# Performance work log

Hardware: AMD Instinct MI355X
Metric: run time of the kernel (lower is better)

The kernel has to match this reference:

```python
import jax, jax.numpy as jnp
import numpy as np

B, N_VEC, N_DIM, N_W, N_HID, VOCAB, N_CLASS = 16, 2048, 32, 4, 128, 32000, 10


def setup_inputs() -> dict:
    key = jax.random.key(0)
    ks = jax.random.split(key, 8)
    data = jax.random.randint(ks[0], (B, N_VEC), 0, VOCAB, dtype=jnp.int64)
    emb = jax.random.normal(ks[1], (VOCAB, N_DIM), dtype=jnp.float32) * 0.1
    # stacked per-layer weights for the n_W WModules: Linear(n_dim->n_hid), GELU, Linear(n_hid->n_vec)
    fw1 = jax.random.normal(ks[2], (N_W, N_DIM, N_HID), dtype=jnp.float32) * (1.0 / np.sqrt(N_DIM))
    fb1 = jnp.zeros((N_W, N_HID), dtype=jnp.float32)
    fw2 = jax.random.normal(ks[3], (N_W, N_HID, N_VEC), dtype=jnp.float32) * (1.0 / np.sqrt(N_HID))
    fb2 = jnp.zeros((N_W, N_VEC), dtype=jnp.float32)
    Wf = jax.random.normal(ks[4], (N_VEC * N_DIM, N_CLASS), dtype=jnp.float32) * (1.0 / np.sqrt(N_VEC * N_DIM))
    bf = jnp.zeros((N_CLASS,), dtype=jnp.float32)
    return {"data": data, "emb": emb, "fw1": fw1, "fb1": fb1, "fw2": fw2, "fb2": fb2, "Wf": Wf, "bf": bf}


def reference(data, emb, fw1, fb1, fw2, fb2, Wf, bf):
    X = emb[data]                       # [B, n_vec, n_dim]
    V = X                               # g is identity (with_g=False)
    # iterate over self.fs[::-1]: indices n_W-1 .. 0
    for i in range(N_W - 1, -1, -1):
        h = jax.nn.gelu(jnp.einsum('bnd,dh->bnh', X, fw1[i]) + fb1[i], approximate=False)
        W = jnp.einsum('bnh,hm->bnm', h, fw2[i]) + fb2[i]   # [B, n_vec, n_vec]
        V = jnp.einsum('bnm,bmd->bnd', W, V)                # [B, n_vec, n_dim]
    out = V.reshape(V.shape[0], -1) @ Wf + bf               # [B, n_class]
    return out
```

## Files before the change

### kernel.cpp

```cpp
#include <hip/hip_runtime.h>

#define NB 16
#define NVEC 2048
#define NDIM 32
#define NW 4
#define NHID 128
#define NCLASS 10
#define NG 32
#define USIZE (129 * 32)

__device__ __forceinline__ float gelu_fast(float x) {
    float t = 1.5957691216057308f * x * (1.0f + 0.044715f * x * x);
    return x / (1.0f + __expf(-t));
}

__device__ __forceinline__ void upart_phase(const float* __restrict__ vs,
                                            const float* __restrict__ fw2s,
                                            const float* __restrict__ fb2l,
                                            int n0, int tid,
                                            float* __restrict__ Up) {
    int kg = tid & 31, d0 = (tid >> 5) * 4;
    float acc[4][4];
#pragma unroll
    for (int i = 0; i < 4; ++i)
#pragma unroll
        for (int j = 0; j < 4; ++j) acc[i][j] = 0.f;
#pragma unroll 4
    for (int mm = 0; mm < 64; mm += 4) {
        float4 w[4], v[4];
#pragma unroll
        for (int i = 0; i < 4; ++i)
            w[i] = *(const float4*)&fw2s[(kg + 32 * i) * 68 + mm];
#pragma unroll
        for (int j = 0; j < 4; ++j)
            v[j] = *(const float4*)&vs[(mm + j) * 36 + d0];
#pragma unroll
        for (int i = 0; i < 4; ++i) {
            const float* wf = (const float*)&w[i];
#pragma unroll
            for (int j = 0; j < 4; ++j) {
                float wv = wf[j];
                acc[i][0] += wv * v[j].x; acc[i][1] += wv * v[j].y;
                acc[i][2] += wv * v[j].z; acc[i][3] += wv * v[j].w;
            }
        }
    }
#pragma unroll
    for (int i = 0; i < 4; ++i)
        *(float4*)&Up[(kg + 32 * i) * 32 + d0] =
            make_float4(acc[i][0], acc[i][1], acc[i][2], acc[i][3]);
    if (tid < 32) {
        float ca = 0.f;
#pragma unroll 8
        for (int mm = 0; mm < 64; ++mm)
            ca += fb2l[n0 + mm] * vs[mm * 36 + tid];
        Up[128 * 32 + tid] = ca;
    }
}

__global__ __launch_bounds__(256) void k_emb(const int* __restrict__ data,
                                             const float* __restrict__ emb,
                                             const float* __restrict__ fw2l,
                                             const float* __restrict__ fb2l,
                                             const float* __restrict__ bf,
                                             float* __restrict__ X,
                                             float* __restrict__ Upart,
                                             float* __restrict__ out) {
    __shared__ float vs[64 * 36];
    __shared__ float fw2s[128 * 68];
    int ng = blockIdx.x, b = blockIdx.y, tid = threadIdx.x;
    int n0 = ng * 64;
#pragma unroll
    for (int j = 0; j < 2; ++j) {
        int i = tid + j * 256;
        int r = i >> 3, c4 = (i & 7) * 4;
        int idx = data[b * NVEC + n0 + r];
        float4 v = *(const float4*)&emb[(size_t)idx * NDIM + c4];
        *(float4*)&vs[r * 36 + c4] = v;
        *(float4*)&X[((size_t)b * NVEC + n0 + r) * NDIM + c4] = v;
    }
#pragma unroll
    for (int j = 0; j < 8; ++j) {
        int i = tid + j * 256;
        int k = i >> 4, c4 = (i & 15) * 4;
        *(float4*)&fw2s[k * 68 + c4] =
            *(const float4*)&fw2l[(size_t)k * NVEC + n0 + c4];
    }
    if (ng == 0 && b == 0 && tid < NB * NCLASS)
        out[tid] = bf[tid % NCLASS];
    __syncthreads();
    upart_phase(vs, fw2s, fb2l, n0, tid, Upart + ((size_t)ng * NB + b) * USIZE);
}

__global__ __launch_bounds__(256) void k_Ured(const float* __restrict__ Upart,
                                              float* __restrict__ U) {
    int b = blockIdx.x;
    int i4 = blockIdx.y * 256 + threadIdx.x;
    if (i4 >= USIZE / 4) return;
    float4 s = ((const float4*)(Upart + (size_t)b * USIZE))[i4];
#pragma unroll
    for (int ms = 1; ms < NG; ++ms) {
        float4 v = ((const float4*)(Upart + ((size_t)ms * NB + b) * USIZE))[i4];
        s.x += v.x; s.y += v.y; s.z += v.z; s.w += v.w;
    }
    ((float4*)(U + (size_t)b * USIZE))[i4] = s;
}

template <bool LAST>
__global__ __launch_bounds__(256) void k_apply(const float* __restrict__ X,
                                               const float* __restrict__ fw1l,
                                               const float* __restrict__ fb1l,
                                               const float* __restrict__ U,
                                               const float* __restrict__ fw2n,
                                               const float* __restrict__ fb2n,
                                               float* __restrict__ Upart,
                                               const float* __restrict__ Wf,
                                               float* __restrict__ out) {
    __shared__ float xs[64 * 36];
    __shared__ float w1s[32 * 132];
    __shared__ float hsb[128 * 68];
    __shared__ float Us[USIZE];
    __shared__ float ored[4][NCLASS];
    int ng = blockIdx.x, b = blockIdx.y, tid = threadIdx.x;
    int n0 = ng * 64;

#pragma unroll
    for (int j = 0; j < 2; ++j) {
        int i = tid + j * 256;
        int r = i >> 3, c4 = (i & 7) * 4;
        *(float4*)&xs[r * 36 + c4] =
            *(const float4*)&X[((size_t)b * NVEC + n0 + r) * NDIM + c4];
    }
#pragma unroll
    for (int j = 0; j < 4; ++j) {
        int i = tid + j * 256;
        int d = i >> 5, c4 = (i & 31) * 4;
        *(float4*)&w1s[d * 132 + c4] = *(const float4*)&fw1l[d * NHID + c4];
    }
    for (int i4 = tid; i4 < USIZE / 4; i4 += 256)
        ((float4*)Us)[i4] = ((const float4*)(U + (size_t)b * USIZE))[i4];
    __syncthreads();

    int rg = tid & 31;
    {
        int k0 = (tid >> 5) * 16;
        float acc[2][16];
        {
            float4 bq[4];
#pragma unroll
            for (int q = 0; q < 4; ++q) bq[q] = *(const float4*)&fb1l[k0 + 4 * q];
#pragma unroll
            for (int q = 0; q < 4; ++q) {
                acc[0][4 * q + 0] = bq[q].x; acc[0][4 * q + 1] = bq[q].y;
                acc[0][4 * q + 2] = bq[q].z; acc[0][4 * q + 3] = bq[q].w;
                acc[1][4 * q + 0] = bq[q].x; acc[1][4 * q + 1] = bq[q].y;
                acc[1][4 * q + 2] = bq[q].z; acc[1][4 * q + 3] = bq[q].w;
            }
        }
#pragma unroll 4
        for (int d = 0; d < NDIM; ++d) {
            float x0 = xs[rg * 36 + d];
            float x1 = xs[(rg + 32) * 36 + d];
            const float* wrow = &w1s[d * 132 + k0];
            float4 w0 = *(const float4*)wrow;
            float4 w1 = *(const float4*)(wrow + 4);
            float4 w2 = *(const float4*)(wrow + 8);
            float4 w3 = *(const float4*)(wrow + 12);
            float wk[16] = {w0.x, w0.y, w0.z, w0.w, w1.x, w1.y, w1.z, w1.w,
                            w2.x, w2.y, w2.z, w2.w, w3.x, w3.y, w3.z, w3.w};
#pragma unroll
            for (int j = 0; j < 16; ++j) {
                acc[0][j] += x0 * wk[j];
                acc[1][j] += x1 * wk[j];
            }
        }
#pragma unroll
        for (int r = 0; r < 2; ++r) {
            int row = rg + 32 * r;
#pragma unroll
            for (int q = 0; q < 4; ++q) {
                float4 o;
                o.x = gelu_fast(acc[r][4 * q + 0]);
                o.y = gelu_fast(acc[r][4 * q + 1]);
                o.z = gelu_fast(acc[r][4 * q + 2]);
                o.w = gelu_fast(acc[r][4 * q + 3]);
                *(float4*)&hsb[row * 132 + k0 + 4 * q] = o;
            }
        }
    }
    __syncthreads();

    int dg = (tid >> 5) & 3, kh = tid >> 7;
    int d0 = dg * 8, kb = kh * 64;
    float a[2][8];
#pragma unroll
    for (int r = 0; r < 2; ++r)
#pragma unroll
        for (int j = 0; j < 8; ++j) a[r][j] = 0.f;
#pragma unroll 4
    for (int ks = 0; ks < 64; ks += 4) {
        int kk = kb + ks;
        float4 h0 = *(const float4*)&hsb[rg * 132 + kk];
        float4 h1 = *(const float4*)&hsb[(rg + 32) * 132 + kk];
        float4 u[4][2];
#pragma unroll
        for (int j = 0; j < 4; ++j) {
            u[j][0] = *(const float4*)&Us[(kk + j) * 32 + d0];
            u[j][1] = *(const float4*)&Us[(kk + j) * 32 + d0 + 4];
        }
        const float* hf0 = (const float*)&h0;
        const float* hf1 = (const float*)&h1;
#pragma unroll
        for (int j = 0; j < 4; ++j) {
            float v0 = hf0[j], v1 = hf1[j];
            a[0][0] += v0 * u[j][0].x; a[0][1] += v0 * u[j][0].y;
            a[0][2] += v0 * u[j][0].z; a[0][3] += v0 * u[j][0].w;
            a[0][4] += v0 * u[j][1].x; a[0][5] += v0 * u[j][1].y;
            a[0][6] += v0 * u[j][1].z; a[0][7] += v0 * u[j][1].w;
            a[1][0] += v1 * u[j][0].x; a[1][1] += v1 * u[j][0].y;
            a[1][2] += v1 * u[j][0].z; a[1][3] += v1 * u[j][0].w;
            a[1][4] += v1 * u[j][1].x; a[1][5] += v1 * u[j][1].y;
            a[1][6] += v1 * u[j][1].z; a[1][7] += v1 * u[j][1].w;
        }
    }
    if (kh == 1) {
#pragma unroll
        for (int r = 0; r < 2; ++r) {
            float* p = &xs[(rg + 32 * r) * 36 + d0];
            *(float4*)p       = make_float4(a[r][0], a[r][1], a[r][2], a[r][3]);
            *(float4*)(p + 4) = make_float4(a[r][4], a[r][5], a[r][6], a[r][7]);
        }
    }
    __syncthreads();

    if constexpr (!LAST) {
#pragma unroll
        for (int j = 0; j < 8; ++j) {
            int i = tid + j * 256;
            int k = i >> 4, c4 = (i & 15) * 4;
            *(float4*)&hsb[k * 68 + c4] =
                *(const float4*)&fw2n[(size_t)k * NVEC + n0 + c4];
        }
    }
    if (kh == 0) {
        float4 ub0 = *(const float4*)&Us[128 * 32 + d0];
        float4 ub1 = *(const float4*)&Us[128 * 32 + d0 + 4];
#pragma unroll
        for (int r = 0; r < 2; ++r) {
            float* p = &xs[(rg + 32 * r) * 36 + d0];
            float4 p0 = *(const float4*)p;
            float4 p1 = *(const float4*)(p + 4);
            a[r][0] += p0.x + ub0.x; a[r][1] += p0.y + ub0.y;
            a[r][2] += p0.z + ub0.z; a[r][3] += p0.w + ub0.w;
            a[r][4] += p1.x + ub1.x; a[r][5] += p1.y + ub1.y;
            a[r][6] += p1.z + ub1.z; a[r][7] += p1.w + ub1.w;
            *(float4*)p       = make_float4(a[r][0], a[r][1], a[r][2], a[r][3]);
            *(float4*)(p + 4) = make_float4(a[r][4], a[r][5], a[r][6], a[r][7]);
        }
    }
    __syncthreads();

    if constexpr (!LAST) {
        upart_phase(xs, hsb, fb2n, n0, tid,
                    Upart + ((size_t)ng * NB + b) * USIZE);
    } else {
        float accC[NCLASS];
#pragma unroll
        for (int c = 0; c < NCLASS; ++c) accC[c] = 0.f;
        if (kh == 0) {
#pragma unroll
            for (int r = 0; r < 2; ++r) {
                int nrow = n0 + rg + 32 * r;
#pragma unroll
                for (int dd = 0; dd < 8; ++dd) {
                    float v = a[r][dd];
                    const float2* wr =
                        (const float2*)(Wf + ((size_t)nrow * 32 + d0 + dd) * NCLASS);
#pragma unroll
                    for (int p = 0; p < 5; ++p) {
                        float2 w = wr[p];
                        accC[2 * p]     += v * w.x;
                        accC[2 * p + 1] += v * w.y;
                    }
                }
            }
        }
#pragma unroll
        for (int c = 0; c < NCLASS; ++c)
#pragma unroll
            for (int off = 32; off >= 1; off >>= 1)
                accC[c] += __shfl_down(accC[c], off, 64);
        int w = tid >> 6;
        if ((tid & 63) == 0) {
#pragma unroll
            for (int c = 0; c < NCLASS; ++c) ored[w][c] = accC[c];
        }
        __syncthreads();
        if (tid < NCLASS)
            atomicAdd(&out[b * NCLASS + tid],
                      ored[0][tid] + ored[1][tid] + ored[2][tid] + ored[3][tid]);
    }
}

extern "C" void kernel_launch(void* const* d_in, const int* in_sizes, int n_in,
                              void* d_out, int out_size, void* d_ws, size_t ws_size,
                              hipStream_t stream) {
    const int*   data = (const int*)d_in[0];
    const float* emb  = (const float*)d_in[1];
    const float* fw1  = (const float*)d_in[2];
    const float* fb1  = (const float*)d_in[3];
    const float* fw2  = (const float*)d_in[4];
    const float* fb2  = (const float*)d_in[5];
    const float* Wf   = (const float*)d_in[6];
    const float* bf   = (const float*)d_in[7];
    float* out = (float*)d_out;

    float* X     = (float*)d_ws;
    float* Upart = X + (size_t)NB * NVEC * NDIM;
    float* U     = Upart + (size_t)NG * NB * USIZE;

    k_emb<<<dim3(NG, NB), 256, 0, stream>>>(data, emb, fw2 + 3 * (size_t)NHID * NVEC,
                                            fb2 + 3 * (size_t)NVEC, bf, X, Upart, out);
    k_Ured<<<dim3(NB, 5), 256, 0, stream>>>(Upart, U);

    for (int i = NW - 1; i >= 1; --i) {
        k_apply<false><<<dim3(NG, NB), 256, 0, stream>>>(
            X, fw1 + (size_t)i * NDIM * NHID, fb1 + (size_t)i * NHID, U,
            fw2 + (size_t)(i - 1) * NHID * NVEC, fb2 + (size_t)(i - 1) * NVEC,
            Upart, nullptr, nullptr);
        k_Ured<<<dim3(NB, 5), 256, 0, stream>>>(Upart, U);
    }
    k_apply<true><<<dim3(NG, NB), 256, 0, stream>>>(
        X, fw1, fb1, U, nullptr, nullptr, nullptr, Wf, out);
}
```

Baseline: 176.0 us.

## Reassociate layer chain into independent 129x129 transfer matrices computed in parallel

Exploits the fact that each layer applies W_i = h_i(X) fw2_i, with X fixed, so the product fw2_j·H_{j+1} can be formed as a small 129x129 augmented matrix per layer and batch. All layers are computed in one parallel kernel instead of a serial apply/reduce chain, then composed with a tiny chain kernel before the final layer. This removes the sequential dependency and cuts the launch count, at the price of extra workspace and more FLOPs spent on the 129x129 transfer matrices.

Result: slower. 198.2 us (+12.6%).

```diff
diff --git a/kernel.cpp b/kernel.cpp
--- a/kernel.cpp
+++ b/kernel.cpp
@@ -6,139 +6,311 @@
 #define NW 4
 #define NHID 128
 #define NCLASS 10
-#define NG 32
-#define USIZE (129 * 32)
+#define TPSZ (129 * 132)
+#define TP4  (TPSZ / 4)
+#define USZ  (129 * 32)
+#define U4   (USZ / 4)
 
 __device__ __forceinline__ float gelu_fast(float x) {
     float t = 1.5957691216057308f * x * (1.0f + 0.044715f * x * x);
     return x / (1.0f + __expf(-t));
 }
 
-__device__ __forceinline__ void upart_phase(const float* __restrict__ vs,
-                                            const float* __restrict__ fw2s,
-                                            const float* __restrict__ fb2l,
-                                            int n0, int tid,
-                                            float* __restrict__ Up) {
-    int kg = tid & 31, d0 = (tid >> 5) * 4;
-    float acc[4][4];
-#pragma unroll
-    for (int i = 0; i < 4; ++i)
-#pragma unroll
-        for (int j = 0; j < 4; ++j) acc[i][j] = 0.f;
+__global__ __launch_bounds__(256) void k_big(const int* __restrict__ data,
+                                             const float* __restrict__ emb,
+                                             const float* __restrict__ fw1,
+                                             const float* __restrict__ fb1,
+                                             const float* __restrict__ fw2,
+                                             const float* __restrict__ fb2,
+                                             float* __restrict__ X,
+                                             float* __restrict__ Tpart,
+                                             float* __restrict__ U3part) {
+    __shared__ float hbuf[128 * 132];
+    __shared__ float fb2s[128];
+    int tid = threadIdx.x, bx = blockIdx.x;
+
+    if (bx < 256) {
+        int b = bx >> 4, chunk = bx & 15, m0 = chunk * 128;
+        const float* fw2l = fw2 + 3 * (size_t)NHID * NVEC;
+        float* xs = hbuf;
+#pragma unroll
+        for (int jj = 0; jj < 4; ++jj) {
+            int i4 = tid + jj * 256;
+            int r = i4 >> 3, c4 = (i4 & 7) * 4;
+            int idx = data[b * NVEC + m0 + r];
+            float4 v = *(const float4*)&emb[(size_t)idx * NDIM + c4];
+            *(float4*)&xs[r * 36 + c4] = v;
+            *(float4*)&X[((size_t)b * NVEC + m0 + r) * NDIM + c4] = v;
+        }
+        if (tid < 128) fb2s[tid] = fb2[3 * NVEC + m0 + tid];
+        __syncthreads();
+        int kg = tid & 31, d0 = (tid >> 5) * 4;
+        float acc[4][4];
+#pragma unroll
+        for (int i = 0; i < 4; ++i)
+#pragma unroll
+            for (int q = 0; q < 4; ++q) acc[i][q] = 0.f;
+        for (int mm = 0; mm < 128; mm += 4) {
+            float4 w[4], v[4];
+#pragma unroll
+            for (int i = 0; i < 4; ++i)
+                w[i] = *(const float4*)&fw2l[(size_t)(kg + 32 * i) * NVEC + m0 + mm];
+#pragma unroll
+            for (int q = 0; q < 4; ++q)
+                v[q] = *(const float4*)&xs[(mm + q) * 36 + d0];
+#pragma unroll
+            for (int i = 0; i < 4; ++i) {
+                const float* wf = (const float*)&w[i];
+#pragma unroll
+                for (int q = 0; q < 4; ++q) {
+                    float wv = wf[q];
+                    acc[i][0] += wv * v[q].x; acc[i][1] += wv * v[q].y;
+                    acc[i][2] += wv * v[q].z; acc[i][3] += wv * v[q].w;
+                }
+            }
+        }
+        float* Up = U3part + (size_t)(b * 16 + chunk) * USZ;
+#pragma unroll
+        for (int i = 0; i < 4; ++i)
+            *(float4*)&Up[(kg + 32 * i) * 32 + d0] =
+                make_float4(acc[i][0], acc[i][1], acc[i][2], acc[i][3]);
+        if (tid < 32) {
+            float ca = 0.f;
+#pragma unroll 8
+            for (int mm = 0; mm < 128; ++mm) ca += fb2s[mm] * xs[mm * 36 + tid];
+            Up[128 * 32 + tid] = ca;
+        }
+    } else {
+        int t = bx - 256;
+        int j = t >> 8, rr = t & 255;
+        int b = rr >> 4, chunk = rr & 15, m0 = chunk * 128;
+        const float* w1l  = fw1 + (size_t)(j + 1) * NDIM * NHID;
+        const float* b1l  = fb1 + (size_t)(j + 1) * NHID;
+        const float* fw2l = fw2 + (size_t)j * NHID * NVEC;
+        float* xs  = hbuf;
+        float* w1s = hbuf + 128 * 33;
+#pragma unroll
+        for (int jj = 0; jj < 4; ++jj) {
+            int i4 = tid + jj * 256;
+            int r = i4 >> 3, c4 = (i4 & 7) * 4;
+            int idx = data[b * NVEC + m0 + r];
+            float4 v = *(const float4*)&emb[(size_t)idx * NDIM + c4];
+            xs[r * 33 + c4] = v.x; xs[r * 33 + c4 + 1] = v.y;
+            xs[r * 33 + c4 + 2] = v.z; xs[r * 33 + c4 + 3] = v.w;
+        }
+#pragma unroll
+        for (int jj = 0; jj < 4; ++jj) {
+            int i4 = tid + jj * 256;
+            int d = i4 >> 5, c4 = (i4 & 31) * 4;
+            *(float4*)&w1s[d * 132 + c4] = *(const float4*)&w1l[d * NHID + c4];
+        }
+        if (tid < 128) fb2s[tid] = fb2[(size_t)j * NVEC + m0 + tid];
+        __syncthreads();
+
+        int rg = tid & 31, kg = tid >> 5, k0 = kg * 16;
+        float hr[4][16];
+        {
+            float4 bq[4];
+#pragma unroll
+            for (int q = 0; q < 4; ++q) bq[q] = *(const float4*)&b1l[k0 + 4 * q];
+#pragma unroll
+            for (int i = 0; i < 4; ++i)
+#pragma unroll
+                for (int q = 0; q < 4; ++q) {
+                    hr[i][4 * q]     = bq[q].x; hr[i][4 * q + 1] = bq[q].y;
+                    hr[i][4 * q + 2] = bq[q].z; hr[i][4 * q + 3] = bq[q].w;
+                }
+        }
 #pragma unroll 4
-    for (int mm = 0; mm < 64; mm += 4) {
-        float4 w[4], v[4];
+        for (int d = 0; d < NDIM; ++d) {
+            float xv[4];
+#pragma unroll
+            for (int i = 0; i < 4; ++i) xv[i] = xs[(rg + 32 * i) * 33 + d];
+            const float* wrow = &w1s[d * 132 + k0];
+            float4 w0 = *(const float4*)wrow;
+            float4 w1 = *(const float4*)(wrow + 4);
+            float4 w2 = *(const float4*)(wrow + 8);
+            float4 w3 = *(const float4*)(wrow + 12);
+            float wk[16] = {w0.x, w0.y, w0.z, w0.w, w1.x, w1.y, w1.z, w1.w,
+                            w2.x, w2.y, w2.z, w2.w, w3.x, w3.y, w3.z, w3.w};
+#pragma unroll
+            for (int i = 0; i < 4; ++i)
+#pragma unroll
+                for (int q = 0; q < 16; ++q) hr[i][q] += xv[i] * wk[q];
+        }
+        __syncthreads();
+#pragma unroll
+        for (int i = 0; i < 4; ++i) {
+            int row = rg + 32 * i;
+#pragma unroll
+            for (int q4 = 0; q4 < 4; ++q4) {
+                float4 o;
+                o.x = gelu_fast(hr[i][4 * q4]);     o.y = gelu_fast(hr[i][4 * q4 + 1]);
+                o.z = gelu_fast(hr[i][4 * q4 + 2]); o.w = gelu_fast(hr[i][4 * q4 + 3]);
+                *(float4*)&hbuf[row * 132 + k0 + 4 * q4] = o;
+            }
+            if (kg == 0) hbuf[row * 132 + 128] = 1.0f;
+        }
+        __syncthreads();
+
+        int pg = tid & 31, qg = tid >> 5, q0 = qg * 16;
+        float ta[4][16];
 #pragma unroll
         for (int i = 0; i < 4; ++i)
-            w[i] = *(const float4*)&fw2s[(kg + 32 * i) * 68 + mm];
-#pragma unroll
-        for (int j = 0; j < 4; ++j)
-            v[j] = *(const float4*)&vs[(mm + j) * 36 + d0];
-#pragma unroll
-        for (int i = 0; i < 4; ++i) {
-            const float* wf = (const float*)&w[i];
-#pragma unroll
-            for (int j = 0; j < 4; ++j) {
-                float wv = wf[j];
-                acc[i][0] += wv * v[j].x; acc[i][1] += wv * v[j].y;
-                acc[i][2] += wv * v[j].z; acc[i][3] += wv * v[j].w;
-            }
-        }
-    }
-#pragma unroll
-    for (int i = 0; i < 4; ++i)
-        *(float4*)&Up[(kg + 32 * i) * 32 + d0] =
-            make_float4(acc[i][0], acc[i][1], acc[i][2], acc[i][3]);
-    if (tid < 32) {
-        float ca = 0.f;
+#pragma unroll
+            for (int q = 0; q < 16; ++q) ta[i][q] = 0.f;
+        for (int mt = 0; mt < 128; mt += 8) {
+            float4 wr[4][2];
+#pragma unroll
+            for (int i = 0; i < 4; ++i) {
+                const float* wb = &fw2l[(size_t)(pg + 32 * i) * NVEC + m0 + mt];
+                wr[i][0] = *(const float4*)wb;
+                wr[i][1] = *(const float4*)(wb + 4);
+            }
+#pragma unroll
+            for (int m8 = 0; m8 < 8; ++m8) {
+                const float* hrow = &hbuf[(mt + m8) * 132 + q0];
+                float4 h0 = *(const float4*)hrow;
+                float4 h1 = *(const float4*)(hrow + 4);
+                float4 h2 = *(const float4*)(hrow + 8);
+                float4 h3 = *(const float4*)(hrow + 12);
+                float hv[16] = {h0.x, h0.y, h0.z, h0.w, h1.x, h1.y, h1.z, h1.w,
+                                h2.x, h2.y, h2.z, h2.w, h3.x, h3.y, h3.z, h3.w};
+#pragma unroll
+                for (int i = 0; i < 4; ++i) {
+                    float wv = ((const float*)&wr[i][m8 >> 2])[m8 & 3];
+#pragma unroll
+                    for (int q = 0; q < 16; ++q) ta[i][q] += wv * hv[q];
+                }
+            }
+        }
+        float* Tp = Tpart + (size_t)t * TPSZ;
+#pragma unroll
+        for (int i = 0; i < 4; ++i)
+#pragma unroll
+            for (int q4 = 0; q4 < 4; ++q4)
+                *(float4*)&Tp[(pg + 32 * i) * 132 + q0 + 4 * q4] =
+                    make_float4(ta[i][4 * q4], ta[i][4 * q4 + 1],
+                                ta[i][4 * q4 + 2], ta[i][4 * q4 + 3]);
+        if (tid < 128) {
+            float s = 0.f;
+            const float* wb = &fw2l[(size_t)tid * NVEC + m0];
 #pragma unroll 8
-        for (int mm = 0; mm < 64; ++mm)
-            ca += fb2l[n0 + mm] * vs[mm * 36 + tid];
-        Up[128 * 32 + tid] = ca;
-    }
-}
-
-__global__ __launch_bounds__(256) void k_emb(const int* __restrict__ data,
-                                             const float* __restrict__ emb,
-                                             const float* __restrict__ fw2l,
-                                             const float* __restrict__ fb2l,
-                                             const float* __restrict__ bf,
-                                             float* __restrict__ X,
-                                             float* __restrict__ Upart,
-                                             float* __restrict__ out) {
-    __shared__ float vs[64 * 36];
-    __shared__ float fw2s[128 * 68];
-    int ng = blockIdx.x, b = blockIdx.y, tid = threadIdx.x;
-    int n0 = ng * 64;
-#pragma unroll
-    for (int j = 0; j < 2; ++j) {
-        int i = tid + j * 256;
-        int r = i >> 3, c4 = (i & 7) * 4;
-        int idx = data[b * NVEC + n0 + r];
-        float4 v = *(const float4*)&emb[(size_t)idx * NDIM + c4];
-        *(float4*)&vs[r * 36 + c4] = v;
-        *(float4*)&X[((size_t)b * NVEC + n0 + r) * NDIM + c4] = v;
-    }
-#pragma unroll
-    for (int j = 0; j < 8; ++j) {
-        int i = tid + j * 256;
-        int k = i >> 4, c4 = (i & 15) * 4;
-        *(float4*)&fw2s[k * 68 + c4] =
-            *(const float4*)&fw2l[(size_t)k * NVEC + n0 + c4];
-    }
-    if (ng == 0 && b == 0 && tid < NB * NCLASS)
-        out[tid] = bf[tid % NCLASS];
-    __syncthreads();
-    upart_phase(vs, fw2s, fb2l, n0, tid, Upart + ((size_t)ng * NB + b) * USIZE);
-}
-
-__global__ __launch_bounds__(256) void k_Ured(const float* __restrict__ Upart,
-                                              float* __restrict__ U) {
-    int b = blockIdx.x;
-    int i4 = blockIdx.y * 256 + threadIdx.x;
-    if (i4 >= USIZE / 4) return;
-    float4 s = ((const float4*)(Upart + (size_t)b * USIZE))[i4];
-#pragma unroll
-    for (int ms = 1; ms < NG; ++ms) {
-        float4 v = ((const float4*)(Upart + ((size_t)ms * NB + b) * USIZE))[i4];
-        s.x += v.x; s.y += v.y; s.z += v.z; s.w += v.w;
-    }
-    ((float4*)(U + (size_t)b * USIZE))[i4] = s;
-}
-
-template <bool LAST>
-__global__ __launch_bounds__(256) void k_apply(const float* __restrict__ X,
-                                               const float* __restrict__ fw1l,
-                                               const float* __restrict__ fb1l,
-                                               const float* __restrict__ U,
-                                               const float* __restrict__ fw2n,
-                                               const float* __restrict__ fb2n,
-                                               float* __restrict__ Upart,
+            for (int mm = 0; mm < 128; mm += 4) {
+                float4 wq = *(const float4*)&wb[mm];
+                s += wq.x + wq.y + wq.z + wq.w;
+            }
+            Tp[tid * 132 + 128] = s;
+        }
+        if (tid < 129) {
+            float s = 0.f;
+#pragma unroll 8
+            for (int mm = 0; mm < 128; ++mm) s += fb2s[mm] * hbuf[mm * 132 + tid];
+            Tp[128 * 132 + tid] = s;
+        }
+    }
+}
+
+__global__ __launch_bounds__(256) void k_red(const float* __restrict__ Tpart,
+                                             const float* __restrict__ U3part,
+                                             float* __restrict__ Tfin,
+                                             float* __restrict__ U3fin) {
+    int x = blockIdx.x, y = blockIdx.y, tid = threadIdx.x;
+    if (y < 48) {
+        int i4 = x * 256 + tid;
+        if (i4 >= TP4) return;
+        float4 s = ((const float4*)Tpart)[(size_t)(y * 16) * TP4 + i4];
+#pragma unroll
+        for (int c = 1; c < 16; ++c) {
+            float4 v = ((const float4*)Tpart)[(size_t)(y * 16 + c) * TP4 + i4];
+            s.x += v.x; s.y += v.y; s.z += v.z; s.w += v.w;
+        }
+        ((float4*)Tfin)[(size_t)y * TP4 + i4] = s;
+    } else {
+        int b = y - 48;
+        int i4 = x * 256 + tid;
+        if (i4 >= U4) return;
+        float4 s = ((const float4*)U3part)[(size_t)(b * 16) * U4 + i4];
+#pragma unroll
+        for (int c = 1; c < 16; ++c) {
+            float4 v = ((const float4*)U3part)[(size_t)(b * 16 + c) * U4 + i4];
+            s.x += v.x; s.y += v.y; s.z += v.z; s.w += v.w;
+        }
+        ((float4*)U3fin)[(size_t)b * U4 + i4] = s;
+    }
+}
+
+__global__ __launch_bounds__(256) void k_chain(const float* __restrict__ Tfin,
+                                               const float* __restrict__ U3fin,
+                                               const float* __restrict__ bf,
+                                               float* __restrict__ U0,
+                                               float* __restrict__ out) {
+    __shared__ float Ul[2][129 * 4];
+    int dg = blockIdx.x, b = blockIdx.y, tid = threadIdx.x;
+    int d0 = dg * 4;
+    if (dg == 0 && tid < NCLASS) out[b * NCLASS + tid] = bf[tid];
+    if (tid < 129)
+        *(float4*)&Ul[0][tid * 4] =
+            *(const float4*)&U3fin[(size_t)b * USZ + tid * 32 + d0];
+    int cur = 0;
+    float4 acc = make_float4(0.f, 0.f, 0.f, 0.f);
+    for (int j = 2; j >= 0; --j) {
+        __syncthreads();
+        if (tid < 129) {
+            const float* rowp = Tfin + (size_t)(j * 16 + b) * TPSZ + tid * 132;
+            acc = make_float4(0.f, 0.f, 0.f, 0.f);
+            for (int r4 = 0; r4 < 32; ++r4) {
+                float4 tv = *(const float4*)&rowp[4 * r4];
+                float4 u0 = *(const float4*)&Ul[cur][(4 * r4 + 0) * 4];
+                float4 u1 = *(const float4*)&Ul[cur][(4 * r4 + 1) * 4];
+                float4 u2 = *(const float4*)&Ul[cur][(4 * r4 + 2) * 4];
+                float4 u3 = *(const float4*)&Ul[cur][(4 * r4 + 3) * 4];
+                acc.x += tv.x * u0.x + tv.y * u1.x + tv.z * u2.x + tv.w * u3.x;
+                acc.y += tv.x * u0.y + tv.y * u1.y + tv.z * u2.y + tv.w * u3.y;
+                acc.z += tv.x * u0.z + tv.y * u1.z + tv.z * u2.z + tv.w * u3.z;
+                acc.w += tv.x * u0.w + tv.y * u1.w + tv.z * u2.w + tv.w * u3.w;
+            }
+            float tl = rowp[128];
+            float4 ub = *(const float4*)&Ul[cur][128 * 4];
+            acc.x += tl * ub.x; acc.y += tl * ub.y;
+            acc.z += tl * ub.z; acc.w += tl * ub.w;
+        }
+        __syncthreads();
+        if (tid < 129) *(float4*)&Ul[cur ^ 1][tid * 4] = acc;
+        cur ^= 1;
+    }
+    if (tid < 129)
+        *(float4*)&U0[(size_t)b * USZ + tid * 32 + d0] = acc;
+}
+
+__global__ __launch_bounds__(256) void k_final(const float* __restrict__ X,
+                                               const float* __restrict__ fw1,
+                                               const float* __restrict__ fb1,
+                                               const float* __restrict__ U0,
                                                const float* __restrict__ Wf,
                                                float* __restrict__ out) {
     __shared__ float xs[64 * 36];
     __shared__ float w1s[32 * 132];
-    __shared__ float hsb[128 * 68];
-    __shared__ float Us[USIZE];
+    __shared__ float hs[64 * 132];
+    __shared__ float Us[USZ];
     __shared__ float ored[4][NCLASS];
     int ng = blockIdx.x, b = blockIdx.y, tid = threadIdx.x;
     int n0 = ng * 64;
-
-#pragma unroll
-    for (int j = 0; j < 2; ++j) {
-        int i = tid + j * 256;
-        int r = i >> 3, c4 = (i & 7) * 4;
+#pragma unroll
+    for (int jj = 0; jj < 2; ++jj) {
+        int i4 = tid + jj * 256;
+        int r = i4 >> 3, c4 = (i4 & 7) * 4;
         *(float4*)&xs[r * 36 + c4] =
             *(const float4*)&X[((size_t)b * NVEC + n0 + r) * NDIM + c4];
     }
 #pragma unroll
-    for (int j = 0; j < 4; ++j) {
-        int i = tid + j * 256;
-        int d = i >> 5, c4 = (i & 31) * 4;
-        *(float4*)&w1s[d * 132 + c4] = *(const float4*)&fw1l[d * NHID + c4];
-    }
-    for (int i4 = tid; i4 < USIZE / 4; i4 += 256)
-        ((float4*)Us)[i4] = ((const float4*)(U + (size_t)b * USIZE))[i4];
+    for (int jj = 0; jj < 4; ++jj) {
+        int i4 = tid + jj * 256;
+        int d = i4 >> 5, c4 = (i4 & 31) * 4;
+        *(float4*)&w1s[d * 132 + c4] = *(const float4*)&fw1[d * NHID + c4];
+    }
+    for (int i4 = tid; i4 < U4; i4 += 256)
+        ((float4*)Us)[i4] = ((const float4*)(U0 + (size_t)b * USZ))[i4];
     __syncthreads();
 
     int rg = tid & 31;
@@ -148,12 +320,12 @@
         {
             float4 bq[4];
 #pragma unroll
-            for (int q = 0; q < 4; ++q) bq[q] = *(const float4*)&fb1l[k0 + 4 * q];
+            for (int q = 0; q < 4; ++q) bq[q] = *(const float4*)&fb1[k0 + 4 * q];
 #pragma unroll
             for (int q = 0; q < 4; ++q) {
-                acc[0][4 * q + 0] = bq[q].x; acc[0][4 * q + 1] = bq[q].y;
+                acc[0][4 * q] = bq[q].x; acc[0][4 * q + 1] = bq[q].y;
                 acc[0][4 * q + 2] = bq[q].z; acc[0][4 * q + 3] = bq[q].w;
-                acc[1][4 * q + 0] = bq[q].x; acc[1][4 * q + 1] = bq[q].y;
+                acc[1][4 * q] = bq[q].x; acc[1][4 * q + 1] = bq[q].y;
                 acc[1][4 * q + 2] = bq[q].z; acc[1][4 * q + 3] = bq[q].w;
             }
         }
@@ -169,22 +341,20 @@
             float wk[16] = {w0.x, w0.y, w0.z, w0.w, w1.x, w1.y, w1.z, w1.w,
                             w2.x, w2.y, w2.z, w2.w, w3.x, w3.y, w3.z, w3.w};
 #pragma unroll
-            for (int j = 0; j < 16; ++j) {
-                acc[0][j] += x0 * wk[j];
-                acc[1][j] += x1 * wk[j];
+            for (int q = 0; q < 16; ++q) {
+                acc[0][q] += x0 * wk[q];
+                acc[1][q] += x1 * wk[q];
             }
         }
 #pragma unroll
         for (int r = 0; r < 2; ++r) {
             int row = rg + 32 * r;
 #pragma unroll
-            for (int q = 0; q < 4; ++q) {
+            for (int q4 = 0; q4 < 4; ++q4) {
                 float4 o;
-                o.x = gelu_fast(acc[r][4 * q + 0]);
-                o.y = gelu_fast(acc[r][4 * q + 1]);
-                o.z = gelu_fast(acc[r][4 * q + 2]);
-                o.w = gelu_fast(acc[r][4 * q + 3]);
-                *(float4*)&hsb[row * 132 + k0 + 4 * q] = o;
+                o.x = gelu_fast(acc[r][4 * q4]);     o.y = gelu_fast(acc[r][4 * q4 + 1]);
+                o.z = gelu_fast(acc[r][4 * q4 + 2]); o.w = gelu_fast(acc[r][4 * q4 + 3]);
+                *(float4*)&hs[row * 132 + k0 + 4 * q4] = o;
             }
         }
     }
@@ -196,31 +366,31 @@
 #pragma unroll
     for (int r = 0; r < 2; ++r)
 #pragma unroll
-        for (int j = 0; j < 8; ++j) a[r][j] = 0.f;
+        for (int q = 0; q < 8; ++q) a[r][q] = 0.f;
 #pragma unroll 4
     for (int ks = 0; ks < 64; ks += 4) {
         int kk = kb + ks;
-        float4 h0 = *(const float4*)&hsb[rg * 132 + kk];
-        float4 h1 = *(const float4*)&hsb[(rg + 32) * 132 + kk];
+        float4 h0 = *(const float4*)&hs[rg * 132 + kk];
+        float4 h1 = *(const float4*)&hs[(rg + 32) * 132 + kk];
         float4 u[4][2];
 #pragma unroll
-        for (int j = 0; j < 4; ++j) {
-            u[j][0] = *(const float4*)&Us[(kk + j) * 32 + d0];
-            u[j][1] = *(const float4*)&Us[(kk + j) * 32 + d0 + 4];
+        for (int q = 0; q < 4; ++q) {
+            u[q][0] = *(const float4*)&Us[(kk + q) * 32 + d0];
+            u[q][1] = *(const float4*)&Us[(kk + q) * 32 + d0 + 4];
         }
         const float* hf0 = (const float*)&h0;
         const float* hf1 = (const float*)&h1;
 #pragma unroll
-        for (int j = 0; j < 4; ++j) {
-            float v0 = hf0[j], v1 = hf1[j];
-            a[0][0] += v0 * u[j][0].x; a[0][1] += v0 * u[j][0].y;
-            a[0][2] += v0 * u[j][0].z; a[0][3] += v0 * u[j][0].w;
-            a[0][4] += v0 * u[j][1].x; a[0][5] += v0 * u[j][1].y;
-            a[0][6] += v0 * u[j][1].z; a[0][7] += v0 * u[j][1].w;
-            a[1][0] += v1 * u[j][0].x; a[1][1] += v1 * u[j][0].y;
-            a[1][2] += v1 * u[j][0].z; a[1][3] += v1 * u[j][0].w;
-            a[1][4] += v1 * u[j][1].x; a[1][5] += v1 * u[j][1].y;
-            a[1][6] += v1 * u[j][1].z; a[1][7] += v1 * u[j][1].w;
+        for (int q = 0; q < 4; ++q) {
+            float v0 = hf0[q], v1 = hf1[q];
+            a[0][0] += v0 * u[q][0].x; a[0][1] += v0 * u[q][0].y;
+            a[0][2] += v0 * u[q][0].z; a[0][3] += v0 * u[q][0].w;
+            a[0][4] += v0 * u[q][1].x; a[0][5] += v0 * u[q][1].y;
+            a[0][6] += v0 * u[q][1].z; a[0][7] += v0 * u[q][1].w;
+            a[1][0] += v1 * u[q][0].x; a[1][1] += v1 * u[q][0].y;
+            a[1][2] += v1 * u[q][0].z; a[1][3] += v1 * u[q][0].w;
+            a[1][4] += v1 * u[q][1].x; a[1][5] += v1 * u[q][1].y;
+            a[1][6] += v1 * u[q][1].z; a[1][7] += v1 * u[q][1].w;
         }
     }
     if (kh == 1) {
@@ -232,74 +402,50 @@
         }
     }
     __syncthreads();
-
-    if constexpr (!LAST) {
-#pragma unroll
-        for (int j = 0; j < 8; ++j) {
-            int i = tid + j * 256;
-            int k = i >> 4, c4 = (i & 15) * 4;
-            *(float4*)&hsb[k * 68 + c4] =
-                *(const float4*)&fw2n[(size_t)k * NVEC + n0 + c4];
-        }
-    }
+    float accC[NCLASS];
+#pragma unroll
+    for (int c = 0; c < NCLASS; ++c) accC[c] = 0.f;
     if (kh == 0) {
         float4 ub0 = *(const float4*)&Us[128 * 32 + d0];
         float4 ub1 = *(const float4*)&Us[128 * 32 + d0 + 4];
 #pragma unroll
         for (int r = 0; r < 2; ++r) {
-            float* p = &xs[(rg + 32 * r) * 36 + d0];
+            const float* p = &xs[(rg + 32 * r) * 36 + d0];
             float4 p0 = *(const float4*)p;
             float4 p1 = *(const float4*)(p + 4);
             a[r][0] += p0.x + ub0.x; a[r][1] += p0.y + ub0.y;
             a[r][2] += p0.z + ub0.z; a[r][3] += p0.w + ub0.w;
             a[r][4] += p1.x + ub1.x; a[r][5] += p1.y + ub1.y;
             a[r][6] += p1.z + ub1.z; a[r][7] += p1.w + ub1.w;
-            *(float4*)p       = make_float4(a[r][0], a[r][1], a[r][2], a[r][3]);
-            *(float4*)(p + 4) = make_float4(a[r][4], a[r][5], a[r][6], a[r][7]);
-        }
+            int nrow = n0 + rg + 32 * r;
+#pragma unroll
+            for (int dd = 0; dd < 8; ++dd) {
+                float v = a[r][dd];
+                const float2* wr =
+                    (const float2*)(Wf + ((size_t)nrow * 32 + d0 + dd) * NCLASS);
+#pragma unroll
+                for (int p5 = 0; p5 < 5; ++p5) {
+                    float2 w = wr[p5];
+                    accC[2 * p5]     += v * w.x;
+                    accC[2 * p5 + 1] += v * w.y;
+                }
+            }
+        }
+    }
+#pragma unroll
+    for (int c = 0; c < NCLASS; ++c)
+#pragma unroll
+        for (int off = 32; off >= 1; off >>= 1)
+            accC[c] += __shfl_down(accC[c], off, 64);
+    int w = tid >> 6;
+    if ((tid & 63) == 0) {
+#pragma unroll
+        for (int c = 0; c < NCLASS; ++c) ored[w][c] = accC[c];
     }
     __syncthreads();
-
-    if constexpr (!LAST) {
-        upart_phase(xs, hsb, fb2n, n0, tid,
-                    Upart + ((size_t)ng * NB + b) * USIZE);
-    } else {
-        float accC[NCLASS];
-#pragma unroll
-        for (int c = 0; c < NCLASS; ++c) accC[c] = 0.f;
-        if (kh == 0) {
-#pragma unroll
-            for (int r = 0; r < 2; ++r) {
-                int nrow = n0 + rg + 32 * r;
-#pragma unroll
-                for (int dd = 0; dd < 8; ++dd) {
-                    float v = a[r][dd];
-                    const float2* wr =
-                        (const float2*)(Wf + ((size_t)nrow * 32 + d0 + dd) * NCLASS);
-#pragma unroll
-                    for (int p = 0; p < 5; ++p) {
-                        float2 w = wr[p];
-                        accC[2 * p]     += v * w.x;
-                        accC[2 * p + 1] += v * w.y;
-                    }
-                }
-            }
-        }
-#pragma unroll
-        for (int c = 0; c < NCLASS; ++c)
-#pragma unroll
-            for (int off = 32; off >= 1; off >>= 1)
-                accC[c] += __shfl_down(accC[c], off, 64);
-        int w = tid >> 6;
-        if ((tid & 63) == 0) {
-#pragma unroll
-            for (int c = 0; c < NCLASS; ++c) ored[w][c] = accC[c];
-        }
-        __syncthreads();
-        if (tid < NCLASS)
-            atomicAdd(&out[b * NCLASS + tid],
-                      ored[0][tid] + ored[1][tid] + ored[2][tid] + ored[3][tid]);
-    }
+    if (tid < NCLASS)
+        atomicAdd(&out[b * NCLASS + tid],
+                  ored[0][tid] + ored[1][tid] + ored[2][tid] + ored[3][tid]);
 }
 
 extern "C" void kernel_launch(void* const* d_in, const int* in_sizes, int n_in,
@@ -315,21 +461,15 @@
     const float* bf   = (const float*)d_in[7];
     float* out = (float*)d_out;
 
-    float* X     = (float*)d_ws;
-    float* Upart = X + (size_t)NB * NVEC * NDIM;
-    float* U     = Upart + (size_t)NG * NB * USIZE;
-
-    k_emb<<<dim3(NG, NB), 256, 0, stream>>>(data, emb, fw2 + 3 * (size_t)NHID * NVEC,
-                                            fb2 + 3 * (size_t)NVEC, bf, X, Upart, out);
-    k_Ured<<<dim3(NB, 5), 256, 0, stream>>>(Upart, U);
-
-    for (int i = NW - 1; i >= 1; --i) {
-        k_apply<false><<<dim3(NG, NB), 256, 0, stream>>>(
-            X, fw1 + (size_t)i * NDIM * NHID, fb1 + (size_t)i * NHID, U,
-            fw2 + (size_t)(i - 1) * NHID * NVEC, fb2 + (size_t)(i - 1) * NVEC,
-            Upart, nullptr, nullptr);
-        k_Ured<<<dim3(NB, 5), 256, 0, stream>>>(Upart, U);
-    }
-    k_apply<true><<<dim3(NG, NB), 256, 0, stream>>>(
-        X, fw1, fb1, U, nullptr, nullptr, nullptr, Wf, out);
-}
+    float* X      = (float*)d_ws;
+    float* Tpart  = X + (size_t)NB * NVEC * NDIM;
+    float* U3part = Tpart + (size_t)768 * TPSZ;
+    float* Tfin   = U3part + (size_t)256 * USZ;
+    float* U3fin  = Tfin + (size_t)48 * TPSZ;
+    float* U0     = U3fin + (size_t)NB * USZ;
+
+    k_big<<<1024, 256, 0, stream>>>(data, emb, fw1, fb1, fw2, fb2, X, Tpart, U3part);
+    k_red<<<dim3(17, 64), 256, 0, stream>>>(Tpart, U3part, Tfin, U3fin);
+    k_chain<<<dim3(8, NB), 256, 0, stream>>>(Tfin, U3fin, bf, U0, out);
+    k_final<<<dim3(32, NB), 256, 0, stream>>>(X, fw1, fb1, U0, Wf, out);
+}
```

## Retile U-partial and apply phases with split-K slots and register-held X

Applied to the files above, without the earlier changes.

Splits the upart phase's m-reduction across two thread halves, each writing its own partial slot, so Upart doubles to 64 slots and the reduce kernel sums twice as many slices. The h@U phase is retiled into four k-segments with 4x8 outputs per thread, and their partial results are combined through a two-stage shared-memory reduction that reuses the w1 buffer. X rows are loaded straight into registers instead of shared memory, the final-class reduction uses only wave 0 with direct atomics, and launch bounds request two blocks per SM. The aim is more ILP per thread and better occupancy, at the cost of extra partial-buffer traffic in the reduce kernel and more barriers.

Measured after the change: 300.1 us. +70.4%, slower.

```diff
diff --git a/kernel.cpp b/kernel.cpp
--- a/kernel.cpp
+++ b/kernel.cpp
@@ -7,6 +7,7 @@
 #define NHID 128
 #define NCLASS 10
 #define NG 32
+#define NSLOT (NG * 2)
 #define USIZE (129 * 32)
 
 __device__ __forceinline__ float gelu_fast(float x) {
@@ -18,43 +19,46 @@
                                             const float* __restrict__ fw2s,
                                             const float* __restrict__ fb2l,
                                             int n0, int tid,
-                                            float* __restrict__ Up) {
-    int kg = tid & 31, d0 = (tid >> 5) * 4;
-    float acc[4][4];
-#pragma unroll
-    for (int i = 0; i < 4; ++i)
-#pragma unroll
-        for (int j = 0; j < 4; ++j) acc[i][j] = 0.f;
-#pragma unroll 4
-    for (int mm = 0; mm < 64; mm += 4) {
-        float4 w[4], v[4];
-#pragma unroll
-        for (int i = 0; i < 4; ++i)
-            w[i] = *(const float4*)&fw2s[(kg + 32 * i) * 68 + mm];
-#pragma unroll
-        for (int j = 0; j < 4; ++j)
-            v[j] = *(const float4*)&vs[(mm + j) * 36 + d0];
-#pragma unroll
-        for (int i = 0; i < 4; ++i) {
+                                            float* __restrict__ Up0) {
+    int kg = tid & 15, dg = (tid >> 4) & 7, mh = tid >> 7;
+    int d0 = dg * 4, mb = mh * 32;
+    float* Up = Up0 + (size_t)mh * (NB * USIZE);
+    float acc[8][4];
+#pragma unroll
+    for (int i = 0; i < 8; ++i)
+#pragma unroll
+        for (int q = 0; q < 4; ++q) acc[i][q] = 0.f;
+#pragma unroll
+    for (int mt = mb; mt < mb + 32; mt += 4) {
+        float4 w[8], v[4];
+#pragma unroll
+        for (int i = 0; i < 8; ++i)
+            w[i] = *(const float4*)&fw2s[(kg + 16 * i) * 68 + mt];
+#pragma unroll
+        for (int q = 0; q < 4; ++q)
+            v[q] = *(const float4*)&vs[(mt + q) * 36 + d0];
+#pragma unroll
+        for (int i = 0; i < 8; ++i) {
             const float* wf = (const float*)&w[i];
 #pragma unroll
-            for (int j = 0; j < 4; ++j) {
-                float wv = wf[j];
-                acc[i][0] += wv * v[j].x; acc[i][1] += wv * v[j].y;
-                acc[i][2] += wv * v[j].z; acc[i][3] += wv * v[j].w;
-            }
-        }
-    }
-#pragma unroll
-    for (int i = 0; i < 4; ++i)
-        *(float4*)&Up[(kg + 32 * i) * 32 + d0] =
+            for (int q = 0; q < 4; ++q) {
+                float wv = wf[q];
+                acc[i][0] += wv * v[q].x; acc[i][1] += wv * v[q].y;
+                acc[i][2] += wv * v[q].z; acc[i][3] += wv * v[q].w;
+            }
+        }
+    }
+#pragma unroll
+    for (int i = 0; i < 8; ++i)
+        *(float4*)&Up[(kg + 16 * i) * 32 + d0] =
             make_float4(acc[i][0], acc[i][1], acc[i][2], acc[i][3]);
-    if (tid < 32) {
+    int l32 = tid & 127;
+    if (l32 < 32) {
         float ca = 0.f;
 #pragma unroll 8
-        for (int mm = 0; mm < 64; ++mm)
-            ca += fb2l[n0 + mm] * vs[mm * 36 + tid];
-        Up[128 * 32 + tid] = ca;
+        for (int mm = 0; mm < 32; ++mm)
+            ca += fb2l[n0 + mb + mm] * vs[(mb + mm) * 36 + l32];
+        Up[128 * 32 + l32] = ca;
     }
 }
 
@@ -89,7 +93,8 @@
     if (ng == 0 && b == 0 && tid < NB * NCLASS)
         out[tid] = bf[tid % NCLASS];
     __syncthreads();
-    upart_phase(vs, fw2s, fb2l, n0, tid, Upart + ((size_t)ng * NB + b) * USIZE);
+    upart_phase(vs, fw2s, fb2l, n0, tid,
+                Upart + ((size_t)(ng * 2) * NB + b) * USIZE);
 }
 
 __global__ __launch_bounds__(256) void k_Ured(const float* __restrict__ Upart,
@@ -98,8 +103,8 @@
     int i4 = blockIdx.y * 256 + threadIdx.x;
     if (i4 >= USIZE / 4) return;
     float4 s = ((const float4*)(Upart + (size_t)b * USIZE))[i4];
-#pragma unroll
-    for (int ms = 1; ms < NG; ++ms) {
+#pragma unroll 8
+    for (int ms = 1; ms < NSLOT; ++ms) {
         float4 v = ((const float4*)(Upart + ((size_t)ms * NB + b) * USIZE))[i4];
         s.x += v.x; s.y += v.y; s.z += v.z; s.w += v.w;
     }
@@ -107,198 +112,224 @@
 }
 
 template <bool LAST>
-__global__ __launch_bounds__(256) void k_apply(const float* __restrict__ X,
-                                               const float* __restrict__ fw1l,
-                                               const float* __restrict__ fb1l,
-                                               const float* __restrict__ U,
-                                               const float* __restrict__ fw2n,
-                                               const float* __restrict__ fb2n,
-                                               float* __restrict__ Upart,
-                                               const float* __restrict__ Wf,
-                                               float* __restrict__ out) {
+__global__ __launch_bounds__(256, 2) void k_apply(const float* __restrict__ X,
+                                                  const float* __restrict__ fw1l,
+                                                  const float* __restrict__ fb1l,
+                                                  const float* __restrict__ U,
+                                                  const float* __restrict__ fw2n,
+                                                  const float* __restrict__ fb2n,
+                                                  float* __restrict__ Upart,
+                                                  const float* __restrict__ Wf,
+                                                  float* __restrict__ out) {
     __shared__ float xs[64 * 36];
-    __shared__ float w1s[32 * 132];
+    __shared__ float w1m[4608];
     __shared__ float hsb[128 * 68];
     __shared__ float Us[USIZE];
-    __shared__ float ored[4][NCLASS];
     int ng = blockIdx.x, b = blockIdx.y, tid = threadIdx.x;
     int n0 = ng * 64;
 
 #pragma unroll
-    for (int j = 0; j < 2; ++j) {
-        int i = tid + j * 256;
-        int r = i >> 3, c4 = (i & 7) * 4;
-        *(float4*)&xs[r * 36 + c4] =
-            *(const float4*)&X[((size_t)b * NVEC + n0 + r) * NDIM + c4];
-    }
-#pragma unroll
-    for (int j = 0; j < 4; ++j) {
-        int i = tid + j * 256;
-        int d = i >> 5, c4 = (i & 31) * 4;
-        *(float4*)&w1s[d * 132 + c4] = *(const float4*)&fw1l[d * NHID + c4];
+    for (int jj = 0; jj < 4; ++jj) {
+        int i4 = tid + jj * 256;
+        int d = i4 >> 5, c4 = (i4 & 31) * 4;
+        *(float4*)&w1m[d * 132 + c4] = *(const float4*)&fw1l[d * NHID + c4];
     }
     for (int i4 = tid; i4 < USIZE / 4; i4 += 256)
         ((float4*)Us)[i4] = ((const float4*)(U + (size_t)b * USIZE))[i4];
-    __syncthreads();
-
-    int rg = tid & 31;
+    int rg5 = tid & 31, kg5 = tid >> 5, k0 = kg5 * 16;
+    float xr[2][32];
     {
-        int k0 = (tid >> 5) * 16;
-        float acc[2][16];
+        const float4* X0 = (const float4*)(X + ((size_t)b * NVEC + n0 + rg5) * NDIM);
+        const float4* X1 = (const float4*)(X + ((size_t)b * NVEC + n0 + rg5 + 32) * NDIM);
+#pragma unroll
+        for (int j = 0; j < 8; ++j) {
+            float4 v0 = X0[j], v1 = X1[j];
+            xr[0][4 * j] = v0.x; xr[0][4 * j + 1] = v0.y;
+            xr[0][4 * j + 2] = v0.z; xr[0][4 * j + 3] = v0.w;
+            xr[1][4 * j] = v1.x; xr[1][4 * j + 1] = v1.y;
+            xr[1][4 * j + 2] = v1.z; xr[1][4 * j + 3] = v1.w;
+        }
+    }
+    __syncthreads();
+
+    {
+        float hacc[2][16];
         {
             float4 bq[4];
 #pragma unroll
             for (int q = 0; q < 4; ++q) bq[q] = *(const float4*)&fb1l[k0 + 4 * q];
 #pragma unroll
             for (int q = 0; q < 4; ++q) {
-                acc[0][4 * q + 0] = bq[q].x; acc[0][4 * q + 1] = bq[q].y;
-                acc[0][4 * q + 2] = bq[q].z; acc[0][4 * q + 3] = bq[q].w;
-                acc[1][4 * q + 0] = bq[q].x; acc[1][4 * q + 1] = bq[q].y;
-                acc[1][4 * q + 2] = bq[q].z; acc[1][4 * q + 3] = bq[q].w;
-            }
-        }
-#pragma unroll 4
+                hacc[0][4 * q] = bq[q].x; hacc[0][4 * q + 1] = bq[q].y;
+                hacc[0][4 * q + 2] = bq[q].z; hacc[0][4 * q + 3] = bq[q].w;
+                hacc[1][4 * q] = bq[q].x; hacc[1][4 * q + 1] = bq[q].y;
+                hacc[1][4 * q + 2] = bq[q].z; hacc[1][4 * q + 3] = bq[q].w;
+            }
+        }
+#pragma unroll
         for (int d = 0; d < NDIM; ++d) {
-            float x0 = xs[rg * 36 + d];
-            float x1 = xs[(rg + 32) * 36 + d];
-            const float* wrow = &w1s[d * 132 + k0];
+            const float* wrow = &w1m[d * 132 + k0];
             float4 w0 = *(const float4*)wrow;
             float4 w1 = *(const float4*)(wrow + 4);
             float4 w2 = *(const float4*)(wrow + 8);
             float4 w3 = *(const float4*)(wrow + 12);
             float wk[16] = {w0.x, w0.y, w0.z, w0.w, w1.x, w1.y, w1.z, w1.w,
                             w2.x, w2.y, w2.z, w2.w, w3.x, w3.y, w3.z, w3.w};
-#pragma unroll
-            for (int j = 0; j < 16; ++j) {
-                acc[0][j] += x0 * wk[j];
-                acc[1][j] += x1 * wk[j];
+            float x0 = xr[0][d], x1 = xr[1][d];
+#pragma unroll
+            for (int q = 0; q < 16; ++q) {
+                hacc[0][q] += x0 * wk[q];
+                hacc[1][q] += x1 * wk[q];
             }
         }
 #pragma unroll
         for (int r = 0; r < 2; ++r) {
-            int row = rg + 32 * r;
+            int row = rg5 + 32 * r;
+#pragma unroll
+            for (int q4 = 0; q4 < 4; ++q4) {
+                float4 o;
+                o.x = gelu_fast(hacc[r][4 * q4]);     o.y = gelu_fast(hacc[r][4 * q4 + 1]);
+                o.z = gelu_fast(hacc[r][4 * q4 + 2]); o.w = gelu_fast(hacc[r][4 * q4 + 3]);
+                *(float4*)&hsb[row * 132 + k0 + 4 * q4] = o;
+            }
+        }
+    }
+    __syncthreads();
+
+    int rg = tid & 15, dg = (tid >> 4) & 3, kseg = tid >> 6;
+    int d0 = dg * 8, kb = kseg * 32;
+    float a[4][8];
+#pragma unroll
+    for (int i = 0; i < 4; ++i)
+#pragma unroll
+        for (int q = 0; q < 8; ++q) a[i][q] = 0.f;
+#pragma unroll
+    for (int ks = kb; ks < kb + 32; ks += 4) {
+        float4 h[4];
+#pragma unroll
+        for (int i = 0; i < 4; ++i)
+            h[i] = *(const float4*)&hsb[(rg + 16 * i) * 132 + ks];
+        float4 u[4][2];
+#pragma unroll
+        for (int q = 0; q < 4; ++q) {
+            u[q][0] = *(const float4*)&Us[(ks + q) * 32 + d0];
+            u[q][1] = *(const float4*)&Us[(ks + q) * 32 + d0 + 4];
+        }
+#pragma unroll
+        for (int i = 0; i < 4; ++i) {
+            const float* hf = (const float*)&h[i];
 #pragma unroll
             for (int q = 0; q < 4; ++q) {
-                float4 o;
-                o.x = gelu_fast(acc[r][4 * q + 0]);
-                o.y = gelu_fast(acc[r][4 * q + 1]);
-                o.z = gelu_fast(acc[r][4 * q + 2]);
-                o.w = gelu_fast(acc[r][4 * q + 3]);
-                *(float4*)&hsb[row * 132 + k0 + 4 * q] = o;
-            }
-        }
-    }
-    __syncthreads();
-
-    int dg = (tid >> 5) & 3, kh = tid >> 7;
-    int d0 = dg * 8, kb = kh * 64;
-    float a[2][8];
-#pragma unroll
-    for (int r = 0; r < 2; ++r)
-#pragma unroll
-        for (int j = 0; j < 8; ++j) a[r][j] = 0.f;
-#pragma unroll 4
-    for (int ks = 0; ks < 64; ks += 4) {
-        int kk = kb + ks;
-        float4 h0 = *(const float4*)&hsb[rg * 132 + kk];
-        float4 h1 = *(const float4*)&hsb[(rg + 32) * 132 + kk];
-        float4 u[4][2];
-#pragma unroll
-        for (int j = 0; j < 4; ++j) {
-            u[j][0] = *(const float4*)&Us[(kk + j) * 32 + d0];
-            u[j][1] = *(const float4*)&Us[(kk + j) * 32 + d0 + 4];
-        }
-        const float* hf0 = (const float*)&h0;
-        const float* hf1 = (const float*)&h1;
-#pragma unroll
-        for (int j = 0; j < 4; ++j) {
-            float v0 = hf0[j], v1 = hf1[j];
-            a[0][0] += v0 * u[j][0].x; a[0][1] += v0 * u[j][0].y;
-            a[0][2] += v0 * u[j][0].z; a[0][3] += v0 * u[j][0].w;
-            a[0][4] += v0 * u[j][1].x; a[0][5] += v0 * u[j][1].y;
-            a[0][6] += v0 * u[j][1].z; a[0][7] += v0 * u[j][1].w;
-            a[1][0] += v1 * u[j][0].x; a[1][1] += v1 * u[j][0].y;
-            a[1][2] += v1 * u[j][0].z; a[1][3] += v1 * u[j][0].w;
-            a[1][4] += v1 * u[j][1].x; a[1][5] += v1 * u[j][1].y;
-            a[1][6] += v1 * u[j][1].z; a[1][7] += v1 * u[j][1].w;
-        }
-    }
-    if (kh == 1) {
-#pragma unroll
-        for (int r = 0; r < 2; ++r) {
-            float* p = &xs[(rg + 32 * r) * 36 + d0];
-            *(float4*)p       = make_float4(a[r][0], a[r][1], a[r][2], a[r][3]);
-            *(float4*)(p + 4) = make_float4(a[r][4], a[r][5], a[r][6], a[r][7]);
-        }
-    }
-    __syncthreads();
-
+                float hv = hf[q];
+                a[i][0] += hv * u[q][0].x; a[i][1] += hv * u[q][0].y;
+                a[i][2] += hv * u[q][0].z; a[i][3] += hv * u[q][0].w;
+                a[i][4] += hv * u[q][1].x; a[i][5] += hv * u[q][1].y;
+                a[i][6] += hv * u[q][1].z; a[i][7] += hv * u[q][1].w;
+            }
+        }
+    }
+    __syncthreads();
+    float* mb0 = w1m;
+    float* mb1 = w1m + 2304;
+    if (kseg == 1) {
+#pragma unroll
+        for (int i = 0; i < 4; ++i) {
+            float* p = &mb0[(rg + 16 * i) * 36 + d0];
+            *(float4*)p       = make_float4(a[i][0], a[i][1], a[i][2], a[i][3]);
+            *(float4*)(p + 4) = make_float4(a[i][4], a[i][5], a[i][6], a[i][7]);
+        }
+    } else if (kseg == 3) {
+#pragma unroll
+        for (int i = 0; i < 4; ++i) {
+            float* p = &mb1[(rg + 16 * i) * 36 + d0];
+            *(float4*)p       = make_float4(a[i][0], a[i][1], a[i][2], a[i][3]);
+            *(float4*)(p + 4) = make_float4(a[i][4], a[i][5], a[i][6], a[i][7]);
+        }
+    }
+    __syncthreads();
     if constexpr (!LAST) {
 #pragma unroll
-        for (int j = 0; j < 8; ++j) {
-            int i = tid + j * 256;
-            int k = i >> 4, c4 = (i & 15) * 4;
+        for (int jj = 0; jj < 8; ++jj) {
+            int i4 = tid + jj * 256;
+            int k = i4 >> 4, c4 = (i4 & 15) * 4;
             *(float4*)&hsb[k * 68 + c4] =
                 *(const float4*)&fw2n[(size_t)k * NVEC + n0 + c4];
         }
     }
-    if (kh == 0) {
+    if (kseg == 0) {
+#pragma unroll
+        for (int i = 0; i < 4; ++i) {
+            const float* p = &mb0[(rg + 16 * i) * 36 + d0];
+            float4 p0 = *(const float4*)p, p1 = *(const float4*)(p + 4);
+            a[i][0] += p0.x; a[i][1] += p0.y; a[i][2] += p0.z; a[i][3] += p0.w;
+            a[i][4] += p1.x; a[i][5] += p1.y; a[i][6] += p1.z; a[i][7] += p1.w;
+        }
+    } else if (kseg == 2) {
+#pragma unroll
+        for (int i = 0; i < 4; ++i) {
+            float* p = &mb1[(rg + 16 * i) * 36 + d0];
+            float4 p0 = *(const float4*)p, p1 = *(const float4*)(p + 4);
+            a[i][0] += p0.x; a[i][1] += p0.y; a[i][2] += p0.z; a[i][3] += p0.w;
+            a[i][4] += p1.x; a[i][5] += p1.y; a[i][6] += p1.z; a[i][7] += p1.w;
+            *(float4*)p       = make_float4(a[i][0], a[i][1], a[i][2], a[i][3]);
+            *(float4*)(p + 4) = make_float4(a[i][4], a[i][5], a[i][6], a[i][7]);
+        }
+    }
+    __syncthreads();
+    if (kseg == 0) {
         float4 ub0 = *(const float4*)&Us[128 * 32 + d0];
         float4 ub1 = *(const float4*)&Us[128 * 32 + d0 + 4];
 #pragma unroll
-        for (int r = 0; r < 2; ++r) {
-            float* p = &xs[(rg + 32 * r) * 36 + d0];
-            float4 p0 = *(const float4*)p;
-            float4 p1 = *(const float4*)(p + 4);
-            a[r][0] += p0.x + ub0.x; a[r][1] += p0.y + ub0.y;
-            a[r][2] += p0.z + ub0.z; a[r][3] += p0.w + ub0.w;
-            a[r][4] += p1.x + ub1.x; a[r][5] += p1.y + ub1.y;
-            a[r][6] += p1.z + ub1.z; a[r][7] += p1.w + ub1.w;
-            *(float4*)p       = make_float4(a[r][0], a[r][1], a[r][2], a[r][3]);
-            *(float4*)(p + 4) = make_float4(a[r][4], a[r][5], a[r][6], a[r][7]);
-        }
-    }
-    __syncthreads();
-
-    if constexpr (!LAST) {
-        upart_phase(xs, hsb, fb2n, n0, tid,
-                    Upart + ((size_t)ng * NB + b) * USIZE);
-    } else {
+        for (int i = 0; i < 4; ++i) {
+            const float* p = &mb1[(rg + 16 * i) * 36 + d0];
+            float4 p0 = *(const float4*)p, p1 = *(const float4*)(p + 4);
+            a[i][0] += p0.x + ub0.x; a[i][1] += p0.y + ub0.y;
+            a[i][2] += p0.z + ub0.z; a[i][3] += p0.w + ub0.w;
+            a[i][4] += p1.x + ub1.x; a[i][5] += p1.y + ub1.y;
+            a[i][6] += p1.z + ub1.z; a[i][7] += p1.w + ub1.w;
+            if constexpr (!LAST) {
+                float* pv = &xs[(rg + 16 * i) * 36 + d0];
+                *(float4*)pv       = make_float4(a[i][0], a[i][1], a[i][2], a[i][3]);
+                *(float4*)(pv + 4) = make_float4(a[i][4], a[i][5], a[i][6], a[i][7]);
+            }
+        }
+    }
+    if constexpr (LAST) {
         float accC[NCLASS];
 #pragma unroll
         for (int c = 0; c < NCLASS; ++c) accC[c] = 0.f;
-        if (kh == 0) {
-#pragma unroll
-            for (int r = 0; r < 2; ++r) {
-                int nrow = n0 + rg + 32 * r;
+        if (kseg == 0) {
+#pragma unroll
+            for (int i = 0; i < 4; ++i) {
+                int nrow = n0 + rg + 16 * i;
 #pragma unroll
                 for (int dd = 0; dd < 8; ++dd) {
-                    float v = a[r][dd];
+                    float v = a[i][dd];
                     const float2* wr =
                         (const float2*)(Wf + ((size_t)nrow * 32 + d0 + dd) * NCLASS);
 #pragma unroll
-                    for (int p = 0; p < 5; ++p) {
-                        float2 w = wr[p];
-                        accC[2 * p]     += v * w.x;
-                        accC[2 * p + 1] += v * w.y;
+                    for (int p5 = 0; p5 < 5; ++p5) {
+                        float2 w = wr[p5];
+                        accC[2 * p5]     += v * w.x;
+                        accC[2 * p5 + 1] += v * w.y;
                     }
                 }
             }
-        }
-#pragma unroll
-        for (int c = 0; c < NCLASS; ++c)
-#pragma unroll
-            for (int off = 32; off >= 1; off >>= 1)
-                accC[c] += __shfl_down(accC[c], off, 64);
-        int w = tid >> 6;
-        if ((tid & 63) == 0) {
-#pragma unroll
-            for (int c = 0; c < NCLASS; ++c) ored[w][c] = accC[c];
-        }
+#pragma unroll
+            for (int c = 0; c < NCLASS; ++c)
+#pragma unroll
+                for (int off = 32; off >= 1; off >>= 1)
+                    accC[c] += __shfl_down(accC[c], off, 64);
+            if (tid == 0) {
+#pragma unroll
+                for (int c = 0; c < NCLASS; ++c)
+                    atomicAdd(&out[b * NCLASS + c], accC[c]);
+            }
+        }
+    } else {
         __syncthreads();
-        if (tid < NCLASS)
-            atomicAdd(&out[b * NCLASS + tid],
-                      ored[0][tid] + ored[1][tid] + ored[2][tid] + ored[3][tid]);
+        upart_phase(xs, hsb, fb2n, n0, tid,
+                    Upart + ((size_t)(ng * 2) * NB + b) * USIZE);
     }
 }
 
@@ -317,7 +348,7 @@
 
     float* X     = (float*)d_ws;
     float* Upart = X + (size_t)NB * NVEC * NDIM;
-    float* U     = Upart + (size_t)NG * NB * USIZE;
+    float* U     = Upart + (size_t)NSLOT * NB * USIZE;
 
     k_emb<<<dim3(NG, NB), 256, 0, stream>>>(data, emb, fw2 + 3 * (size_t)NHID * NVEC,
                                             fb2 + 3 * (size_t)NVEC, bf, X, Upart, out);
```
